# Kernel tuning notes

Measured on AMD Instinct MI355X. Metric: run time of the kernel, lower is better.

## Reference

```python
import jax, jax.numpy as jnp
import numpy as np

D_MODEL = 1024
NUM_HEADS = 16
D_HEAD = D_MODEL // NUM_HEADS


def setup_inputs() -> dict:
    key = jax.random.key(0)
    ks = jax.random.split(key, 9)
    s = 1.0 / np.sqrt(D_MODEL)
    return {
        "x": jax.random.normal(ks[0], (4, 2048, D_MODEL), dtype=jnp.float32),
        "Wq": jax.random.normal(ks[1], (D_MODEL, D_MODEL), dtype=jnp.float32) * s,
        "bq": jnp.zeros((D_MODEL,), dtype=jnp.float32),
        "Wk": jax.random.normal(ks[2], (D_MODEL, D_MODEL), dtype=jnp.float32) * s,
        "bk": jnp.zeros((D_MODEL,), dtype=jnp.float32),
        "Wv": jax.random.normal(ks[3], (D_MODEL, D_MODEL), dtype=jnp.float32) * s,
        "bv": jnp.zeros((D_MODEL,), dtype=jnp.float32),
        "Wo": jax.random.normal(ks[4], (D_MODEL, D_MODEL), dtype=jnp.float32) * s,
        "bo": jnp.zeros((D_MODEL,), dtype=jnp.float32),
    }


def reference(x, Wq, bq, Wk, bk, Wv, bv, Wo, bo):
    B, S, _ = x.shape
    # projections (torch Linear: y = x @ W^T + b; here W stored as [in, out])
    q = (x @ Wq + bq).reshape(B, S, NUM_HEADS, D_HEAD).transpose(0, 2, 1, 3)
    k = (x @ Wk + bk).reshape(B, S, NUM_HEADS, D_HEAD).transpose(0, 2, 1, 3)
    v = (x @ Wv + bv).reshape(B, S, NUM_HEADS, D_HEAD).transpose(0, 2, 1, 3)
    scale = 1.0 / jnp.sqrt(jnp.asarray(D_HEAD, dtype=x.dtype))
    scores = jnp.einsum("bhqd,bhkd->bhqk", q, k) * scale  # [B,H,S,S]
    attn = jax.nn.softmax(scores, axis=-1)
    ctx = jnp.einsum("bhqk,bhkd->bhqd", attn, v)  # [B,H,S,Dh]
    ctx = ctx.transpose(0, 2, 1, 3).reshape(B, S, D_MODEL)
    return ctx @ Wo + bo
```

## Files before the change

### kernel.cpp

```cpp
#include <hip/hip_runtime.h>
#include <hip/hip_bf16.h>

#define DM 1024
#define NH 16
#define DH 64
#define BB 4
#define SS 2048
#define MROWS (BB*SS)

typedef unsigned short u16;
typedef short bf16x8 __attribute__((ext_vector_type(8)));
typedef short bf16x4 __attribute__((ext_vector_type(4)));
typedef float f32x4 __attribute__((ext_vector_type(4)));
typedef unsigned uintx2 __attribute__((ext_vector_type(2)));

#define MFMA16(a, b, c) __builtin_amdgcn_mfma_f32_16x16x32_bf16((a), (b), (c), 0, 0, 0)
#define MFMA16K16(a, b, c) __builtin_amdgcn_mfma_f32_16x16x16bf16_1k((a), (b), (c), 0, 0, 0)

__device__ __forceinline__ u16 f2bf(float f) {
  union { float f; unsigned u; } v; v.f = f;
  unsigned u = v.u;
  return (u16)((u + 0x7fffu + ((u >> 16) & 1u)) >> 16);
}

__device__ __forceinline__ unsigned pack2bf(float a, float b) {
  __hip_bfloat162 h = __float22bfloat162_rn(make_float2(a, b));
  unsigned u;
  __builtin_memcpy(&u, &h, 4);
  return u;
}

__device__ __forceinline__ bf16x8 ld_bf8(const u16* p) {
  return *(const bf16x8*)p;
}

__global__ __launch_bounds__(256) void k_cvt_x(const float* __restrict__ x,
                                               u16* __restrict__ xb) {
  int i = (blockIdx.x * 256 + threadIdx.x) * 4;
  float4 v = *(const float4*)(x + i);
  ushort4 o;
  o.x = f2bf(v.x); o.y = f2bf(v.y); o.z = f2bf(v.z); o.w = f2bf(v.w);
  *(ushort4*)(xb + i) = o;
}

__global__ __launch_bounds__(1024) void k_tw(const float* __restrict__ Wq,
                                             const float* __restrict__ Wk,
                                             const float* __restrict__ Wv,
                                             const float* __restrict__ Wo,
                                             u16* __restrict__ Wt) {
  __shared__ float t[32][33];
  int k0 = blockIdx.x * 32;
  int seg = blockIdx.y >> 5;
  int n0 = (blockIdx.y & 31) * 32;
  const float* W = seg == 0 ? Wq : seg == 1 ? Wk : seg == 2 ? Wv : Wo;
  int tx = threadIdx.x, ty = threadIdx.y;
  t[ty][tx] = W[(size_t)(k0 + ty) * DM + n0 + tx];
  __syncthreads();
  Wt[(size_t)(seg * DM + n0 + ty) * DM + k0 + tx] = f2bf(t[tx][ty]);
}

__global__ __launch_bounds__(256) void k_gemm(
    const u16* __restrict__ A, const u16* __restrict__ Bt,
    int M, int N, int K,
    const float* __restrict__ b0, const float* __restrict__ b1,
    const float* __restrict__ b2,
    u16* __restrict__ oq, u16* __restrict__ ok, u16* __restrict__ ov,
    float* __restrict__ of, int mode) {
  __shared__ __align__(16) u16 As[128 * 32];
  __shared__ __align__(16) u16 Bs[128 * 32];
  int tid = threadIdx.x;
  int wave = tid >> 6, lane = tid & 63, quad = lane >> 4, l16 = lane & 15;
  int bm = blockIdx.x * 128, bn = blockIdx.y * 128;
  int wr = (wave >> 1) * 64, wc = (wave & 1) * 64;
  f32x4 acc[4][4] = {};

  const u16* ga = A + (size_t)(bm + wave * 32 + (lane >> 2)) * K + (lane & 3) * 8;
  const u16* gb = Bt + (size_t)(bn + wave * 32 + (lane >> 2)) * K + (lane & 3) * 8;
  u16* lda = &As[wave * 1024];
  u16* ldb = &Bs[wave * 1024];

  for (int k0 = 0; k0 < K; k0 += 32) {
#pragma unroll
    for (int i = 0; i < 2; ++i) {
      __builtin_amdgcn_global_load_lds(
          (const __attribute__((address_space(1))) void*)(ga + (size_t)i * 16 * K + k0),
          (__attribute__((address_space(3))) void*)(lda + i * 512), 16, 0, 0);
      __builtin_amdgcn_global_load_lds(
          (const __attribute__((address_space(1))) void*)(gb + (size_t)i * 16 * K + k0),
          (__attribute__((address_space(3))) void*)(ldb + i * 512), 16, 0, 0);
    }
    __syncthreads();
    bf16x8 af[4], bfr[4];
#pragma unroll
    for (int mi = 0; mi < 4; ++mi)
      af[mi] = *(const bf16x8*)(&As[(wr + mi * 16 + l16) * 32 + quad * 8]);
#pragma unroll
    for (int ni = 0; ni < 4; ++ni)
      bfr[ni] = *(const bf16x8*)(&Bs[(wc + ni * 16 + l16) * 32 + quad * 8]);
#pragma unroll
    for (int mi = 0; mi < 4; ++mi)
#pragma unroll
      for (int ni = 0; ni < 4; ++ni)
        acc[mi][ni] = MFMA16(af[mi], bfr[ni], acc[mi][ni]);
    __syncthreads();
  }

  if (mode == 0) {
#pragma unroll
    for (int mi = 0; mi < 4; ++mi)
#pragma unroll
      for (int ni = 0; ni < 4; ++ni)
#pragma unroll
        for (int r = 0; r < 4; ++r) {
          int row = bm + wr + mi * 16 + quad * 4 + r;
          int col = bn + wc + ni * 16 + l16;
          of[(size_t)row * N + col] = acc[mi][ni][r] + b0[col];
        }
  } else {
    int seg = bn >> 10;
    const float* bia = seg == 0 ? b0 : seg == 1 ? b1 : b2;
    int cb = bn & 1023;
    if (seg == 2) {
#pragma unroll
      for (int mi = 0; mi < 4; ++mi)
#pragma unroll
        for (int ni = 0; ni < 4; ++ni) {
          int row = bm + wr + mi * 16 + quad * 4;
          int col = cb + wc + ni * 16 + l16;
          float bv_ = bia[col];
          int bb2 = row >> 11, s = row & 2047, hh = col >> 6, dh = col & 63;
          ushort4 o4;
          o4.x = f2bf(acc[mi][ni][0] + bv_);
          o4.y = f2bf(acc[mi][ni][1] + bv_);
          o4.z = f2bf(acc[mi][ni][2] + bv_);
          o4.w = f2bf(acc[mi][ni][3] + bv_);
          *(ushort4*)(&ov[(((size_t)bb2 * NH + hh) * DH + dh) * SS + s]) = o4;
        }
    } else {
      u16* o = seg == 0 ? oq : ok;
      float sc = seg == 0 ? (0.125f * 1.44269504f) : 1.0f;
#pragma unroll
      for (int mi = 0; mi < 4; ++mi)
#pragma unroll
        for (int ni = 0; ni < 4; ++ni)
#pragma unroll
          for (int r = 0; r < 4; ++r) {
            int row = bm + wr + mi * 16 + quad * 4 + r;
            int col = cb + wc + ni * 16 + l16;
            float v = (acc[mi][ni][r] + bia[col]) * sc;
            int bb2 = row >> 11, s = row & 2047, hh = col >> 6, dh = col & 63;
            o[((((size_t)bb2 * NH + hh) * SS) + s) * DH + dh] = f2bf(v);
          }
    }
  }
}

__global__ __launch_bounds__(256) void k_attn(const u16* __restrict__ Q,
                                              const u16* __restrict__ Kg,
                                              const u16* __restrict__ VT,
                                              u16* __restrict__ ctx) {
  __shared__ __align__(16) u16 Ks[2][64][72];
  __shared__ __align__(16) u16 Vts[2][64][72];
  int tid = threadIdx.x;
  int wave = tid >> 6, lane = tid & 63, quad = lane >> 4, l16 = lane & 15;
  int q0 = blockIdx.x * 128;
  int h = blockIdx.y, b = blockIdx.z;
  size_t bh = ((size_t)b * NH + h) * SS * DH;
  const u16* Qp = Q + bh + (size_t)(q0 + wave * 32) * DH;
  const u16* Kp = Kg + bh;
  const u16* Vp = VT + ((size_t)b * NH + h) * DH * SS;

  bf16x8 qf[2][2];
#pragma unroll
  for (int qt = 0; qt < 2; ++qt) {
    qf[qt][0] = ld_bf8(Qp + (qt * 16 + l16) * DH + quad * 8);
    qf[qt][1] = ld_bf8(Qp + (qt * 16 + l16) * DH + 32 + quad * 8);
  }

  f32x4 Ot[4][2] = {};
  float lrun[2] = {0.0f, 0.0f};

  int sr = tid >> 3;
  int sc = (tid & 7) * 8;

  const u16* kfr = &Ks[0][l16][quad * 8];
  const u16* vfr = &Vts[0][l16][0];
  u16* kst = &Ks[0][sr][sc];
  u16* vst = &Vts[0][sr][sc];
  const u16* kg = Kp + (size_t)sr * DH + sc;
  const u16* vg = Vp + (size_t)sr * SS + sc;

#pragma unroll
  for (int i = 0; i < 2; ++i) {
    *(bf16x8*)(kst + i * 2304) = ld_bf8(kg + i * 32 * DH);
    *(bf16x8*)(vst + i * 2304) = ld_bf8(vg + (size_t)i * 32 * SS);
  }
  __syncthreads();

  int kv = 64;

#define ATTN_STEP(P)                                                         \
  {                                                                          \
    f32x4 s[2][4];                                                           \
    _Pragma("unroll") for (int t = 0; t < 4; ++t) {                          \
      bf16x8 kb0 = *(const bf16x8*)(kfr + (P) * 4608 + t * 1152);            \
      bf16x8 kb1 = *(const bf16x8*)(kfr + (P) * 4608 + t * 1152 + 32);       \
      _Pragma("unroll") for (int qt = 0; qt < 2; ++qt) {                     \
        f32x4 z = {};                                                        \
        z = MFMA16(kb0, qf[qt][0], z);                                       \
        z = MFMA16(kb1, qf[qt][1], z);                                       \
        s[qt][t] = z;                                                        \
      }                                                                      \
    }                                                                        \
    if (kv < SS) {                                                           \
      _Pragma("unroll") for (int i = 0; i < 2; ++i) {                        \
        *(bf16x8*)(kst + (1 - (P)) * 4608 + i * 2304) =                      \
            ld_bf8(kg + (size_t)kv * DH + i * 32 * DH);                      \
        *(bf16x8*)(vst + (1 - (P)) * 4608 + i * 2304) =                      \
            ld_bf8(vg + (size_t)i * 32 * SS + kv);                           \
      }                                                                      \
    }                                                                        \
    bf16x4 pb[2][4];                                                         \
    _Pragma("unroll") for (int qt = 0; qt < 2; ++qt)                         \
        _Pragma("unroll") for (int t = 0; t < 4; ++t) {                      \
      float e0 = __builtin_amdgcn_exp2f(s[qt][t][0]);                        \
      float e1 = __builtin_amdgcn_exp2f(s[qt][t][1]);                        \
      float e2 = __builtin_amdgcn_exp2f(s[qt][t][2]);                        \
      float e3 = __builtin_amdgcn_exp2f(s[qt][t][3]);                        \
      lrun[qt] += (e0 + e1) + (e2 + e3);                                     \
      uintx2 w;                                                              \
      w[0] = pack2bf(e0, e1);                                                \
      w[1] = pack2bf(e2, e3);                                                \
      pb[qt][t] = __builtin_bit_cast(bf16x4, w);                             \
    }                                                                        \
    _Pragma("unroll") for (int c = 0; c < 4; ++c)                            \
        _Pragma("unroll") for (int dt = 0; dt < 4; ++dt) {                   \
      bf16x4 va = *(const bf16x4*)(vfr + (P) * 4608 + dt * 1152 + c * 16 +   \
                                   quad * 4);                                \
      _Pragma("unroll") for (int qt = 0; qt < 2; ++qt)                       \
          Ot[dt][qt] = MFMA16K16(va, pb[qt][c], Ot[dt][qt]);                 \
    }                                                                        \
    __syncthreads();                                                         \
    kv += 64;                                                                \
  }

  for (int it = 0; it < SS / 128; ++it) {
    ATTN_STEP(0);
    ATTN_STEP(1);
  }
#undef ATTN_STEP

  float inv[2];
#pragma unroll
  for (int qt = 0; qt < 2; ++qt) {
    float l = lrun[qt];
    l += __shfl_xor(l, 16);
    l += __shfl_xor(l, 32);
    inv[qt] = 1.0f / l;
  }

#pragma unroll
  for (int qt = 0; qt < 2; ++qt) {
    int q = q0 + wave * 32 + qt * 16 + l16;
    size_t ob = ((size_t)b * SS + q) * DM + h * DH;
#pragma unroll
    for (int dt = 0; dt < 4; ++dt) {
      uintx2 o;
      o[0] = pack2bf(Ot[dt][qt][0] * inv[qt], Ot[dt][qt][1] * inv[qt]);
      o[1] = pack2bf(Ot[dt][qt][2] * inv[qt], Ot[dt][qt][3] * inv[qt]);
      *(uintx2*)(&ctx[ob + dt * 16 + quad * 4]) = o;
    }
  }
}

extern "C" void kernel_launch(void* const* d_in, const int* in_sizes, int n_in,
                              void* d_out, int out_size, void* d_ws, size_t ws_size,
                              hipStream_t stream) {
  const float* x  = (const float*)d_in[0];
  const float* Wq = (const float*)d_in[1];
  const float* bq = (const float*)d_in[2];
  const float* Wk = (const float*)d_in[3];
  const float* bk = (const float*)d_in[4];
  const float* Wv = (const float*)d_in[5];
  const float* bv = (const float*)d_in[6];
  const float* Wo = (const float*)d_in[7];
  const float* bo = (const float*)d_in[8];
  float* out = (float*)d_out;

  char* ws = (char*)d_ws;
  u16* xb = (u16*)(ws);
  u16* Wt = (u16*)(ws + (16u << 20));
  u16* Qb = (u16*)(ws + (24u << 20));
  u16* Kb = (u16*)(ws + (40u << 20));
  u16* VT = (u16*)(ws + (56u << 20));
  u16* Cb = (u16*)(ws + (72u << 20));

  k_cvt_x<<<MROWS * DM / 1024, 256, 0, stream>>>(x, xb);
  k_tw<<<dim3(32, 128), dim3(32, 32), 0, stream>>>(Wq, Wk, Wv, Wo, Wt);
  k_gemm<<<dim3(MROWS / 128, 24), 256, 0, stream>>>(
      xb, Wt, MROWS, 3 * DM, DM, bq, bk, bv, Qb, Kb, VT, nullptr, 1);
  k_attn<<<dim3(SS / 128, NH, BB), 256, 0, stream>>>(Qb, Kb, VT, Cb);
  k_gemm<<<dim3(MROWS / 128, 8), 256, 0, stream>>>(
      Cb, Wt + (size_t)3 * DM * DM, MROWS, DM, DM, bo, nullptr, nullptr,
      nullptr, nullptr, nullptr, out, 0);
}
```

Before: 324.4 us.

## Load K/V tiles via direct global-to-LDS DMA with XOR-swizzled layout

Replaces the register-staged K/V tile copies in the attention kernel with global_load_lds direct-to-LDS transfers. The padded LDS layout becomes unpadded with an XOR swizzle on 16-byte chunks, which avoids bank conflicts while fitting the DMA's contiguous per-wave write pattern. The softmax exponentials are also truncated to bf16 with perm instructions instead of rounding, and the row sum now uses the truncated values. This removes VGPR staging and store instructions but changes rounding and relies on the DMA ordering being covered by the existing barriers.

```diff
diff --git a/kernel.cpp b/kernel.cpp
--- a/kernel.cpp
+++ b/kernel.cpp
@@ -159,8 +159,8 @@
                                               const u16* __restrict__ Kg,
                                               const u16* __restrict__ VT,
                                               u16* __restrict__ ctx) {
-  __shared__ __align__(16) u16 Ks[2][64][72];
-  __shared__ __align__(16) u16 Vts[2][64][72];
+  __shared__ __align__(16) u16 Ks[2][64][64];
+  __shared__ __align__(16) u16 Vts[2][64][64];
   int tid = threadIdx.x;
   int wave = tid >> 6, lane = tid & 63, quad = lane >> 4, l16 = lane & 15;
   int q0 = blockIdx.x * 128;
@@ -180,68 +180,100 @@
   f32x4 Ot[4][2] = {};
   float lrun[2] = {0.0f, 0.0f};
 
-  int sr = tid >> 3;
-  int sc = (tid & 7) * 8;
-
-  const u16* kfr = &Ks[0][l16][quad * 8];
-  const u16* vfr = &Vts[0][l16][0];
-  u16* kst = &Ks[0][sr][sc];
-  u16* vst = &Vts[0][sr][sc];
-  const u16* kg = Kp + (size_t)sr * DH + sc;
-  const u16* vg = Vp + (size_t)sr * SS + sc;
-
+  int lrow = lane >> 3;
+  int lcb = (lane & 7) ^ lrow;
+  const u16* kdma[2];
+  const u16* vdma[2];
+  u16* kl[2];
+  u16* vl[2];
 #pragma unroll
   for (int i = 0; i < 2; ++i) {
-    *(bf16x8*)(kst + i * 2304) = ld_bf8(kg + i * 32 * DH);
-    *(bf16x8*)(vst + i * 2304) = ld_bf8(vg + (size_t)i * 32 * SS);
+    int chunk = wave * 2 + i;
+    kdma[i] = Kp + (size_t)(chunk * 8 + lrow) * DH + lcb * 8;
+    vdma[i] = Vp + (size_t)(chunk * 8 + lrow) * SS + lcb * 8;
+    kl[i] = &Ks[0][chunk * 8][0];
+    vl[i] = &Vts[0][chunk * 8][0];
+  }
+
+  int e7 = l16 & 7, qh = quad >> 1, qp = quad & 1;
+  const u16* kfr0 = &Ks[0][l16][(quad ^ e7) * 8];
+  const u16* kfr1 = &Ks[0][l16][((quad + 4) ^ e7) * 8];
+  const u16* vfr[4];
+#pragma unroll
+  for (int c = 0; c < 4; ++c)
+    vfr[c] = &Vts[0][l16][((2 * c + qh) ^ e7) * 8 + qp * 4];
+
+#pragma unroll
+  for (int i = 0; i < 2; ++i) {
+    __builtin_amdgcn_global_load_lds(
+        (const __attribute__((address_space(1))) void*)kdma[i],
+        (__attribute__((address_space(3))) void*)kl[i], 16, 0, 0);
+    __builtin_amdgcn_global_load_lds(
+        (const __attribute__((address_space(1))) void*)vdma[i],
+        (__attribute__((address_space(3))) void*)vl[i], 16, 0, 0);
   }
   __syncthreads();
 
   int kv = 64;
 
-#define ATTN_STEP(P)                                                         \
-  {                                                                          \
-    f32x4 s[2][4];                                                           \
-    _Pragma("unroll") for (int t = 0; t < 4; ++t) {                          \
-      bf16x8 kb0 = *(const bf16x8*)(kfr + (P) * 4608 + t * 1152);            \
-      bf16x8 kb1 = *(const bf16x8*)(kfr + (P) * 4608 + t * 1152 + 32);       \
-      _Pragma("unroll") for (int qt = 0; qt < 2; ++qt) {                     \
-        f32x4 z = {};                                                        \
-        z = MFMA16(kb0, qf[qt][0], z);                                       \
-        z = MFMA16(kb1, qf[qt][1], z);                                       \
-        s[qt][t] = z;                                                        \
-      }                                                                      \
-    }                                                                        \
-    if (kv < SS) {                                                           \
-      _Pragma("unroll") for (int i = 0; i < 2; ++i) {                        \
-        *(bf16x8*)(kst + (1 - (P)) * 4608 + i * 2304) =                      \
-            ld_bf8(kg + (size_t)kv * DH + i * 32 * DH);                      \
-        *(bf16x8*)(vst + (1 - (P)) * 4608 + i * 2304) =                      \
-            ld_bf8(vg + (size_t)i * 32 * SS + kv);                           \
-      }                                                                      \
-    }                                                                        \
-    bf16x4 pb[2][4];                                                         \
-    _Pragma("unroll") for (int qt = 0; qt < 2; ++qt)                         \
-        _Pragma("unroll") for (int t = 0; t < 4; ++t) {                      \
-      float e0 = __builtin_amdgcn_exp2f(s[qt][t][0]);                        \
-      float e1 = __builtin_amdgcn_exp2f(s[qt][t][1]);                        \
-      float e2 = __builtin_amdgcn_exp2f(s[qt][t][2]);                        \
-      float e3 = __builtin_amdgcn_exp2f(s[qt][t][3]);                        \
-      lrun[qt] += (e0 + e1) + (e2 + e3);                                     \
-      uintx2 w;                                                              \
-      w[0] = pack2bf(e0, e1);                                                \
-      w[1] = pack2bf(e2, e3);                                                \
-      pb[qt][t] = __builtin_bit_cast(bf16x4, w);                             \
-    }                                                                        \
-    _Pragma("unroll") for (int c = 0; c < 4; ++c)                            \
-        _Pragma("unroll") for (int dt = 0; dt < 4; ++dt) {                   \
-      bf16x4 va = *(const bf16x4*)(vfr + (P) * 4608 + dt * 1152 + c * 16 +   \
-                                   quad * 4);                                \
-      _Pragma("unroll") for (int qt = 0; qt < 2; ++qt)                       \
-          Ot[dt][qt] = MFMA16K16(va, pb[qt][c], Ot[dt][qt]);                 \
-    }                                                                        \
-    __syncthreads();                                                         \
-    kv += 64;                                                                \
+#define ATTN_STEP(P)                                                          \
+  {                                                                           \
+    f32x4 s[2][4];                                                            \
+    _Pragma("unroll") for (int t = 0; t < 4; ++t) {                           \
+      bf16x8 kb0 = *(const bf16x8*)(kfr0 + (P) * 4096 + t * 1024);            \
+      bf16x8 kb1 = *(const bf16x8*)(kfr1 + (P) * 4096 + t * 1024);            \
+      _Pragma("unroll") for (int qt = 0; qt < 2; ++qt) {                      \
+        f32x4 z = {};                                                         \
+        z = MFMA16(kb0, qf[qt][0], z);                                        \
+        z = MFMA16(kb1, qf[qt][1], z);                                        \
+        s[qt][t] = z;                                                         \
+      }                                                                       \
+    }                                                                         \
+    if (kv < SS) {                                                            \
+      _Pragma("unroll") for (int i = 0; i < 2; ++i) {                         \
+        __builtin_amdgcn_global_load_lds(                                     \
+            (const __attribute__((address_space(1))) void*)(kdma[i] +         \
+                                                            (size_t)kv * DH), \
+            (__attribute__((address_space(3))) void*)(kl[i] +                 \
+                                                      (1 - (P)) * 4096),      \
+            16, 0, 0);                                                        \
+        __builtin_amdgcn_global_load_lds(                                     \
+            (const __attribute__((address_space(1))) void*)(vdma[i] + kv),    \
+            (__attribute__((address_space(3))) void*)(vl[i] +                 \
+                                                      (1 - (P)) * 4096),      \
+            16, 0, 0);                                                        \
+      }                                                                       \
+    }                                                                         \
+    bf16x4 pb[2][4];                                                          \
+    _Pragma("unroll") for (int qt = 0; qt < 2; ++qt)                          \
+        _Pragma("unroll") for (int t = 0; t < 4; ++t) {                       \
+      unsigned u0 = __builtin_bit_cast(                                       \
+          unsigned, __builtin_amdgcn_exp2f(s[qt][t][0]));                     \
+      unsigned u1 = __builtin_bit_cast(                                       \
+          unsigned, __builtin_amdgcn_exp2f(s[qt][t][1]));                     \
+      unsigned u2 = __builtin_bit_cast(                                       \
+          unsigned, __builtin_amdgcn_exp2f(s[qt][t][2]));                     \
+      unsigned u3 = __builtin_bit_cast(                                       \
+          unsigned, __builtin_amdgcn_exp2f(s[qt][t][3]));                     \
+      unsigned w0 = __builtin_amdgcn_perm(u1, u0, 0x07060302u);               \
+      unsigned w1 = __builtin_amdgcn_perm(u3, u2, 0x07060302u);               \
+      lrun[qt] += __builtin_bit_cast(float, w0 << 16) +                       \
+                  __builtin_bit_cast(float, w0 & 0xffff0000u) +               \
+                  __builtin_bit_cast(float, w1 << 16) +                       \
+                  __builtin_bit_cast(float, w1 & 0xffff0000u);                \
+      uintx2 w;                                                               \
+      w[0] = w0;                                                              \
+      w[1] = w1;                                                              \
+      pb[qt][t] = __builtin_bit_cast(bf16x4, w);                              \
+    }                                                                         \
+    _Pragma("unroll") for (int c = 0; c < 4; ++c)                             \
+        _Pragma("unroll") for (int dt = 0; dt < 4; ++dt) {                    \
+      bf16x4 va = *(const bf16x4*)(vfr[c] + (P) * 4096 + dt * 1024);          \
+      _Pragma("unroll") for (int qt = 0; qt < 2; ++qt)                        \
+          Ot[dt][qt] = MFMA16K16(va, pb[qt][c], Ot[dt][qt]);                  \
+    }                                                                         \
+    __syncthreads();                                                          \
+    kv += 64;                                                                 \
   }
 
   for (int it = 0; it < SS / 128; ++it) {
```

Measured after the change: 316.4 us. -2.5%, faster.
